# Kernel optimization log

Measured on AMD Instinct MI355X. Metric: run time of the kernel, lower is better.

## Reference

```python
import jax, jax.numpy as jnp
import numpy as np

N = 16384
F_IN = 256
F_OUT = 256


def setup_inputs() -> dict:
    key = jax.random.key(0)
    k1, k2, k3 = jax.random.split(key, 3)
    x = jax.random.normal(k1, (N, F_IN), dtype=jnp.float32)
    # dense 0/1 adjacency (original masks with adj[j] == 1)
    adj = jax.random.randint(k2, (N, N), 0, 2, dtype=jnp.int32)
    # glorot-uniform init for weight [2F_in, F_out]
    stdv = np.sqrt(6.0 / (2 * F_IN + F_OUT)).astype(np.float32)
    weight = jax.random.uniform(k3, (2 * F_IN, F_OUT), dtype=jnp.float32,
                                minval=-stdv, maxval=stdv)
    bias = jnp.zeros((F_OUT,), dtype=jnp.float32)
    return {"x": x, "adj": adj, "weight": weight, "bias": bias}


def reference(x, adj, weight, bias):
    # Mean over neighbors (adj row == 1): segment-mean expressed as a
    # normalized dense matmul -- equivalent to the per-row boolean-mask mean.
    a = adj.astype(x.dtype)                      # [N, N]
    deg = jnp.sum(a, axis=1, keepdims=True)      # [N, 1]
    x1 = (a @ x) / deg                           # [N, F] neighbor mean
    n_x = jnp.concatenate([x1, x], axis=1)       # [N, 2F]
    return n_x @ weight + bias                   # [N, F_out]
```

## Files before the change

### kernel.cpp

```cpp
#include <hip/hip_runtime.h>
#include <hip/hip_bf16.h>
#include <stdint.h>


typedef short bf16x8 __attribute__((ext_vector_type(8)));
typedef float f32x4  __attribute__((ext_vector_type(4)));

__device__ __forceinline__ uint32_t pack_bf16_rne(float lo, float hi) {
    uint32_t ul = __float_as_uint(lo);
    uint32_t uh = __float_as_uint(hi);
    ul = (ul + 0x7fffu + ((ul >> 16) & 1u)) >> 16;
    uh = (uh + 0x7fffu + ((uh >> 16) & 1u)) >> 16;
    return ul | (uh << 16);
}

__global__ __launch_bounds__(256) void k_transpose_w(const float* __restrict__ w,
                                                     uint16_t* __restrict__ wt) {
    int idx = blockIdx.x * 256 + threadIdx.x;
    int n = idx >> 8;
    int k = idx & 255;
    int row = (n < 256) ? k : (256 + k);
    int col = (n < 256) ? n : (n - 256);
    uint32_t u = __float_as_uint(w[row * 256 + col]);
    u = (u + 0x7fffu + ((u >> 16) & 1u)) >> 16;
    wt[idx] = (uint16_t)u;
}

__global__ __launch_bounds__(256) void k_small_gemm(const float* __restrict__ x,
                                                    const uint16_t* __restrict__ wt,
                                                    const float* __restrict__ bias,
                                                    uint16_t* __restrict__ yT,
                                                    float* __restrict__ z) {
    __shared__ uint16_t As[128 * 32];
    __shared__ uint16_t Bs[128 * 32];

    const int t  = threadIdx.x;
    const int ct = blockIdx.x;
    const int rt = blockIdx.y;
    const int m0 = rt * 128;
    const int n0 = ct * 128;

    const int lane = t & 63, w = t >> 6;
    const int wr = w >> 1, wc = w & 1;
    const int l15 = lane & 15, quad = lane >> 4;

    f32x4 acc[4][4] = {};

    float4 a_reg[4];
    uint4  b_reg[2];

#pragma unroll
    for (int i = 0; i < 4; ++i) {
        int f4 = t + 256 * i, row = f4 >> 3, c4 = f4 & 7;
        a_reg[i] = *(const float4*)(x + (m0 + row) * 256 + c4 * 4);
    }
#pragma unroll
    for (int i = 0; i < 2; ++i) {
        int u4 = t + 256 * i, n_l = u4 >> 2, part = u4 & 3;
        b_reg[i] = *(const uint4*)(wt + (n0 + n_l) * 256 + part * 8);
    }

    for (int kk = 0; kk < 8; ++kk) {
        __syncthreads();
#pragma unroll
        for (int i = 0; i < 4; ++i) {
            int f4 = t + 256 * i, row = f4 >> 3, c4 = f4 & 7;
            uint2 p;
            p.x = pack_bf16_rne(a_reg[i].x, a_reg[i].y);
            p.y = pack_bf16_rne(a_reg[i].z, a_reg[i].w);
            *(uint2*)(As + row * 32 + c4 * 4) = p;
        }
#pragma unroll
        for (int i = 0; i < 2; ++i) {
            int u4 = t + 256 * i, n_l = u4 >> 2, part = u4 & 3;
            *(uint4*)(Bs + n_l * 32 + part * 8) = b_reg[i];
        }
        if (kk < 7) {
            int k0 = (kk + 1) * 32;
#pragma unroll
            for (int i = 0; i < 4; ++i) {
                int f4 = t + 256 * i, row = f4 >> 3, c4 = f4 & 7;
                a_reg[i] = *(const float4*)(x + (m0 + row) * 256 + k0 + c4 * 4);
            }
#pragma unroll
            for (int i = 0; i < 2; ++i) {
                int u4 = t + 256 * i, n_l = u4 >> 2, part = u4 & 3;
                b_reg[i] = *(const uint4*)(wt + (n0 + n_l) * 256 + k0 + part * 8);
            }
        }
        __syncthreads();

        bf16x8 a_frag[4], b_frag[4];
#pragma unroll
        for (int fr = 0; fr < 4; ++fr)
            a_frag[fr] = *(const bf16x8*)(As + (wr * 64 + fr * 16 + l15) * 32 + quad * 8);
#pragma unroll
        for (int fc = 0; fc < 4; ++fc)
            b_frag[fc] = *(const bf16x8*)(Bs + (wc * 64 + fc * 16 + l15) * 32 + quad * 8);
#pragma unroll
        for (int fr = 0; fr < 4; ++fr)
#pragma unroll
            for (int fc = 0; fc < 4; ++fc)
                acc[fr][fc] = __builtin_amdgcn_mfma_f32_16x16x32_bf16(
                    a_frag[fr], b_frag[fc], acc[fr][fc], 0, 0, 0);
    }

    if (ct < 2) {
#pragma unroll
        for (int fr = 0; fr < 4; ++fr) {
            int m_base = m0 + wr * 64 + fr * 16 + quad * 4;
#pragma unroll
            for (int fc = 0; fc < 4; ++fc) {
                int n_g = n0 + wc * 64 + fc * 16 + l15;
                uint2 pp;
                pp.x = pack_bf16_rne(acc[fr][fc][0], acc[fr][fc][1]);
                pp.y = pack_bf16_rne(acc[fr][fc][2], acc[fr][fc][3]);
                *(uint2*)(yT + (size_t)n_g * 16384 + m_base) = pp;
            }
        }
    } else {
#pragma unroll
        for (int fr = 0; fr < 4; ++fr) {
            int m_base = m0 + wr * 64 + fr * 16 + quad * 4;
#pragma unroll
            for (int fc = 0; fc < 4; ++fc) {
                int n_g = (n0 - 256) + wc * 64 + fc * 16 + l15;
                float bv = bias[n_g];
#pragma unroll
                for (int r = 0; r < 4; ++r)
                    z[(size_t)(m_base + r) * 256 + n_g] = acc[fr][fc][r] + bv;
            }
        }
    }
}

__global__ __launch_bounds__(512) void k_big_gemm(const int* __restrict__ adj,
                                                  const uint16_t* __restrict__ yT,
                                                  const float* __restrict__ z,
                                                  float* __restrict__ out) {
    __shared__ uint16_t As[64 * 32];
    __shared__ uint16_t Bs[256 * 32];
    __shared__ int degs[64];

    const int t = threadIdx.x;
    const int m0 = blockIdx.x * 64;
    const int lane = t & 63, w = t >> 6;
    const int wr = w >> 2, wc = w & 3;
    const int l15 = lane & 15, quad = lane >> 4;

    f32x4 acc[2][4] = {};

    const int a_row = t >> 3, a_c4 = t & 7;
    const int4* pa = (const int4*)(adj + (size_t)(m0 + a_row) * 16384) + a_c4;
    uint16_t* As_w = As + a_row * 32 + a_c4 * 4;

    const int b_n = t >> 2, b_part = t & 3;
    const uint4* pb0 = (const uint4*)yT + (size_t)b_n * 2048 + b_part;
    const uint4* pb1 = pb0 + (size_t)128 * 2048;
    uint16_t* Bs_w0 = Bs + b_n * 32 + b_part * 8;
    uint16_t* Bs_w1 = Bs_w0 + 128 * 32;

    int4 a_reg = *pa; pa += 8;
    uint4 b_reg0 = *pb0; pb0 += 4;
    uint4 b_reg1 = *pb1; pb1 += 4;
    int degp = 0;

    for (int kk = 0; kk < 512; ++kk) {
        __syncthreads();
        degp += a_reg.x + a_reg.y + a_reg.z + a_reg.w;
        uint2 p;
        p.x = (uint32_t)(a_reg.x | (a_reg.y << 16)) * 0x3F80u;
        p.y = (uint32_t)(a_reg.z | (a_reg.w << 16)) * 0x3F80u;
        *(uint2*)As_w = p;
        *(uint4*)Bs_w0 = b_reg0;
        *(uint4*)Bs_w1 = b_reg1;
        if (kk < 511) {
            a_reg = *pa; pa += 8;
            b_reg0 = *pb0; pb0 += 4;
            b_reg1 = *pb1; pb1 += 4;
        }
        __syncthreads();

        bf16x8 a_frag[2], b_frag[4];
#pragma unroll
        for (int fr = 0; fr < 2; ++fr)
            a_frag[fr] = *(const bf16x8*)(As + (wr * 32 + fr * 16 + l15) * 32 + quad * 8);
#pragma unroll
        for (int fc = 0; fc < 4; ++fc)
            b_frag[fc] = *(const bf16x8*)(Bs + (wc * 64 + fc * 16 + l15) * 32 + quad * 8);
#pragma unroll
        for (int fr = 0; fr < 2; ++fr)
#pragma unroll
            for (int fc = 0; fc < 4; ++fc)
                acc[fr][fc] = __builtin_amdgcn_mfma_f32_16x16x32_bf16(
                    a_frag[fr], b_frag[fc], acc[fr][fc], 0, 0, 0);
    }

    degp += __shfl_down(degp, 4);
    degp += __shfl_down(degp, 2);
    degp += __shfl_down(degp, 1);
    if ((t & 7) == 0) degs[t >> 3] = degp;
    __syncthreads();

#pragma unroll
    for (int fr = 0; fr < 2; ++fr) {
#pragma unroll
        for (int r = 0; r < 4; ++r) {
            int m_l = wr * 32 + fr * 16 + quad * 4 + r;
            float inv = 1.0f / (float)degs[m_l];
            size_t mrow = (size_t)(m0 + m_l) * 256;
#pragma unroll
            for (int fc = 0; fc < 4; ++fc) {
                int n_g = wc * 64 + fc * 16 + l15;
                out[mrow + n_g] = acc[fr][fc][r] * inv + z[mrow + n_g];
            }
        }
    }
}

extern "C" void kernel_launch(void* const* d_in, const int* in_sizes, int n_in,
                              void* d_out, int out_size, void* d_ws, size_t ws_size,
                              hipStream_t stream) {
    const float* x      = (const float*)d_in[0];
    const int*   adj    = (const int*)d_in[1];
    const float* weight = (const float*)d_in[2];
    const float* bias   = (const float*)d_in[3];
    float* out = (float*)d_out;

    uint16_t* wt = (uint16_t*)d_ws;
    uint16_t* yT = (uint16_t*)((char*)d_ws + 262144);
    float*    z  = (float*)((char*)d_ws + 262144 + 8388608);

    k_transpose_w<<<512, 256, 0, stream>>>(weight, wt);
    k_small_gemm<<<dim3(4, 128), 256, 0, stream>>>(x, wt, bias, yT, z);
    k_big_gemm<<<256, 512, 0, stream>>>(adj, yT, z, out);
}
```

Baseline: 1.600 ms.

## Double-buffer big GEMM LDS with direct global-to-LDS loads and swizzle

Rewrites the main adjacency GEMM loop to double-buffer both LDS tiles, so there is one barrier per k-step instead of two. The yT tile now goes straight from global memory to LDS with global_load_lds, using an XOR swizzle on the column chunk to cut bank conflicts. The A tile gets a padded stride of 40. Launch bounds request two blocks per CU, which doubles LDS use and may limit registers.

New measurement: 1.719 ms. 7.5% more time.

```diff
diff --git a/kernel.cpp b/kernel.cpp
--- a/kernel.cpp
+++ b/kernel.cpp
@@ -12,6 +12,12 @@
     ul = (ul + 0x7fffu + ((ul >> 16) & 1u)) >> 16;
     uh = (uh + 0x7fffu + ((uh >> 16) & 1u)) >> 16;
     return ul | (uh << 16);
+}
+
+__device__ __forceinline__ void gload_lds16(const void* g, void* l) {
+    __builtin_amdgcn_global_load_lds(
+        (__attribute__((address_space(1))) void*)g,
+        (__attribute__((address_space(3))) void*)l, 16, 0, 0);
 }
 
 __global__ __launch_bounds__(256) void k_transpose_w(const float* __restrict__ w,
@@ -134,12 +140,15 @@
     }
 }
 
-__global__ __launch_bounds__(512) void k_big_gemm(const int* __restrict__ adj,
-                                                  const uint16_t* __restrict__ yT,
-                                                  const float* __restrict__ z,
-                                                  float* __restrict__ out) {
-    __shared__ uint16_t As[64 * 32];
-    __shared__ uint16_t Bs[256 * 32];
+#define A_STRIDE 40
+#define A_SZ (64 * A_STRIDE)
+#define B_SZ (256 * 32)
+__global__ __launch_bounds__(512, 2) void k_big_gemm(const int* __restrict__ adj,
+                                                     const uint16_t* __restrict__ yT,
+                                                     const float* __restrict__ z,
+                                                     float* __restrict__ out) {
+    __shared__ uint16_t As_f[2 * A_SZ];
+    __shared__ uint16_t Bs_f[2 * B_SZ];
     __shared__ int degs[64];
 
     const int t = threadIdx.x;
@@ -150,56 +159,84 @@
 
     f32x4 acc[2][4] = {};
 
-    const int a_row = t >> 3, a_c4 = t & 7;
-    const int4* pa = (const int4*)(adj + (size_t)(m0 + a_row) * 16384) + a_c4;
-    uint16_t* As_w = As + a_row * 32 + a_c4 * 4;
-
-    const int b_n = t >> 2, b_part = t & 3;
-    const uint4* pb0 = (const uint4*)yT + (size_t)b_n * 2048 + b_part;
-    const uint4* pb1 = pb0 + (size_t)128 * 2048;
-    uint16_t* Bs_w0 = Bs + b_n * 32 + b_part * 8;
-    uint16_t* Bs_w1 = Bs_w0 + 128 * 32;
-
-    int4 a_reg = *pa; pa += 8;
-    uint4 b_reg0 = *pb0; pb0 += 4;
-    uint4 b_reg1 = *pb1; pb1 += 4;
-    int degp = 0;
+    const int a_n = t >> 3, a_c4 = t & 7;
+    const int4* pa4 = (const int4*)(adj + (size_t)(m0 + a_n) * 16384) + a_c4;
+    const int a_lds = a_n * A_STRIDE + a_c4 * 4;
+
+    const uint16_t* pbg[2];
+    int b_ldsbase[2];
+#pragma unroll
+    for (int i = 0; i < 2; ++i) {
+        int base = (w * 2 + i) * 64;
+        int s = base + lane;
+        int bn = s >> 2;
+        int bc = (s & 3) ^ ((bn >> 1) & 3);
+        pbg[i] = yT + (size_t)bn * 16384 + bc * 8;
+        b_ldsbase[i] = base * 8;
+    }
+
+#pragma unroll
+    for (int i = 0; i < 2; ++i) {
+        gload_lds16(pbg[i], &Bs_f[b_ldsbase[i]]);
+        pbg[i] += 32;
+    }
+    int4 a = pa4[0]; pa4 += 8;
+    int degp = a.x + a.y + a.z + a.w;
+    {
+        uint2 pv;
+        pv.x = (uint32_t)(a.x | (a.y << 16)) * 0x3F80u;
+        pv.y = (uint32_t)(a.z | (a.w << 16)) * 0x3F80u;
+        *(uint2*)&As_f[a_lds] = pv;
+    }
+    __syncthreads();
 
     for (int kk = 0; kk < 512; ++kk) {
-        __syncthreads();
-        degp += a_reg.x + a_reg.y + a_reg.z + a_reg.w;
-        uint2 p;
-        p.x = (uint32_t)(a_reg.x | (a_reg.y << 16)) * 0x3F80u;
-        p.y = (uint32_t)(a_reg.z | (a_reg.w << 16)) * 0x3F80u;
-        *(uint2*)As_w = p;
-        *(uint4*)Bs_w0 = b_reg0;
-        *(uint4*)Bs_w1 = b_reg1;
+        const int p = kk & 1;
+        int4 an;
         if (kk < 511) {
-            a_reg = *pa; pa += 8;
-            b_reg0 = *pb0; pb0 += 4;
-            b_reg1 = *pb1; pb1 += 4;
-        }
-        __syncthreads();
-
-        bf16x8 a_frag[2], b_frag[4];
-#pragma unroll
-        for (int fr = 0; fr < 2; ++fr)
-            a_frag[fr] = *(const bf16x8*)(As + (wr * 32 + fr * 16 + l15) * 32 + quad * 8);
-#pragma unroll
-        for (int fc = 0; fc < 4; ++fc)
-            b_frag[fc] = *(const bf16x8*)(Bs + (wc * 64 + fc * 16 + l15) * 32 + quad * 8);
+            an = pa4[0]; pa4 += 8;
+#pragma unroll
+            for (int i = 0; i < 2; ++i) {
+                gload_lds16(pbg[i], &Bs_f[(1 - p) * B_SZ + b_ldsbase[i]]);
+                pbg[i] += 32;
+            }
+        }
+
+        const uint16_t* Ar = As_f + p * A_SZ;
+        const uint16_t* Br = Bs_f + p * B_SZ;
+        bf16x8 af[2], bfr[4];
+#pragma unroll
+        for (int fr = 0; fr < 2; ++fr) {
+            int row = wr * 32 + fr * 16 + l15;
+            af[fr] = *(const bf16x8*)(Ar + row * A_STRIDE + quad * 8);
+        }
+#pragma unroll
+        for (int fc = 0; fc < 4; ++fc) {
+            int n = wc * 64 + fc * 16 + l15;
+            int cs = quad ^ ((n >> 1) & 3);
+            bfr[fc] = *(const bf16x8*)(Br + n * 32 + cs * 8);
+        }
 #pragma unroll
         for (int fr = 0; fr < 2; ++fr)
 #pragma unroll
             for (int fc = 0; fc < 4; ++fc)
                 acc[fr][fc] = __builtin_amdgcn_mfma_f32_16x16x32_bf16(
-                    a_frag[fr], b_frag[fc], acc[fr][fc], 0, 0, 0);
+                    af[fr], bfr[fc], acc[fr][fc], 0, 0, 0);
+
+        if (kk < 511) {
+            degp += an.x + an.y + an.z + an.w;
+            uint2 pv;
+            pv.x = (uint32_t)(an.x | (an.y << 16)) * 0x3F80u;
+            pv.y = (uint32_t)(an.z | (an.w << 16)) * 0x3F80u;
+            *(uint2*)&As_f[(1 - p) * A_SZ + a_lds] = pv;
+        }
+        __syncthreads();
     }
 
     degp += __shfl_down(degp, 4);
     degp += __shfl_down(degp, 2);
     degp += __shfl_down(degp, 1);
-    if ((t & 7) == 0) degs[t >> 3] = degp;
+    if ((t & 7) == 0) degs[a_n] = degp;
     __syncthreads();
 
 #pragma unroll
```
